# Kernel tuning notes

Hardware: AMD Instinct MI355X
Metric: run time of the kernel (lower is better)

## Reference

```python
import jax, jax.numpy as jnp
import numpy as np

N_Q = 6        # qubits per circuit
N_CL = 32      # entangler layers per circuit
N_MOD = 32     # number of qlayer modules (feature parts)
PART = 64      # 2048 // 32

# Pauli-Z sign table: state flattened as (B, 2**N_Q) with wire 0 the most
# significant axis; signs[k, i] = (-1)**bit_i(k).
_bits = (np.arange(2 ** N_Q)[:, None] >> np.arange(N_Q - 1, -1, -1)[None, :]) & 1
SIGNS = jnp.asarray(1.0 - 2.0 * _bits, dtype=jnp.float32)  # [64, 6]


def _apply_1q(state, gate, wire):
    # state: [B, 2, 2, 2, 2, 2, 2] complex64; gate: [2, 2]
    axis = 1 + wire
    state = jnp.tensordot(gate, state, axes=((1,), (axis,)))
    return jnp.moveaxis(state, 0, axis)


def _apply_cnot(state, ctrl, tgt):
    ci, ti = 1 + ctrl, 1 + tgt
    s0 = jax.lax.index_in_dim(state, 0, ci, keepdims=True)
    s1 = jax.lax.index_in_dim(state, 1, ci, keepdims=True)
    return jnp.concatenate([s0, jnp.flip(s1, axis=ti)], axis=ci)


def _rx(theta):
    c = jnp.cos(theta * 0.5).astype(jnp.complex64)
    s = jnp.sin(theta * 0.5).astype(jnp.complex64)
    return jnp.stack([jnp.stack([c, -1j * s]), jnp.stack([-1j * s, c])])


def _circuit(angles, weights):
    # angles: [B, 6] (AngleEmbedding RY params); weights: [N_CL, 6] (RX params)
    B = angles.shape[0]
    half = angles * 0.5
    # RY(a)|0> = cos(a/2)|0> + sin(a/2)|1>  -> product state
    amps = jnp.stack([jnp.cos(half), jnp.sin(half)], axis=-1).astype(jnp.complex64)  # [B,6,2]
    state = amps[:, 0]
    for q in range(1, N_Q):
        state = state[..., None] * amps[:, q].reshape((B,) + (1,) * q + (2,))
    # state: [B,2,2,2,2,2,2]

    def layer(st, w):
        # BasicEntanglerLayers: RX on every wire, then ring of CNOTs
        for q in range(N_Q):
            st = _apply_1q(st, _rx(w[q]), q)
        for q in range(N_Q):
            st = _apply_cnot(st, q, (q + 1) % N_Q)
        return st, None

    state, _ = jax.lax.scan(jax.checkpoint(layer), state, weights)
    probs = (state.real ** 2 + state.imag ** 2).reshape(B, 2 ** N_Q)
    return probs @ SIGNS  # [B, 6] expvals of PauliZ on each wire


def _forward(features, Wp, bp, qw, Wf, bf):
    B = features.shape[0]
    parts = features.reshape(B, N_MOD, PART)                 # 32 chunks of 64
    angles = jnp.einsum('bpd,qd->bpq', parts, Wp) + bp       # shared projector -> [B,32,6]
    outs = jax.vmap(_circuit, in_axes=(1, 0), out_axes=1)(angles, qw)  # [B,32,6]
    return outs.reshape(B, N_MOD * N_Q) @ Wf.T + bf          # [B, num_classes]


def setup_inputs() -> dict:
    key = jax.random.key(0)
    k1, k2, k3, k4 = jax.random.split(key, 4)
    B, num_classes = 2048, 150
    features = jax.random.normal(k1, (B, 2048), dtype=jnp.float32)
    Wp = jax.random.normal(k2, (N_Q, PART), dtype=jnp.float32) * (1.0 / np.sqrt(PART))
    bp = jnp.zeros((N_Q,), dtype=jnp.float32)
    qw = jax.random.uniform(k3, (N_MOD, N_CL, N_Q), dtype=jnp.float32) * (2.0 * np.pi)
    Wf = jax.random.normal(k4, (num_classes, N_MOD * N_Q), dtype=jnp.float32) * (1.0 / np.sqrt(N_MOD * N_Q))
    bf = jnp.zeros((num_classes,), dtype=jnp.float32)
    return {'features': features, 'Wp': Wp, 'bp': bp, 'qw': qw, 'Wf': Wf, 'bf': bf}


def reference(features, Wp, bp, qw, Wf, bf):
    return _forward(features, Wp, bp, qw, Wf, bf)
```

## Files before the change

kernel.cpp:

```cpp
#include <hip/hip_runtime.h>

#define NQ   6
#define DIM  64
#define NMOD 32
#define NCL  32
#define BATCH 2048
#define NCLS 150
#define KF   192
#define NROWS (BATCH*NMOD)

#define OFF_UT    0
#define OFF_OUTS  262144

__global__ __launch_bounds__(256) void k_prep(const float* __restrict__ qw,
                                              float* __restrict__ UTf) {
    __shared__ float2 csl[NCL * NQ];
    int tid = threadIdx.x;
    int lane = tid & 63;
    int w = tid >> 6;
    int p = blockIdx.x >> 4;
    int col = ((blockIdx.x & 15) << 2) + w;

    if (tid < NCL * NQ) {
        float s, c;
        sincosf(0.5f * qw[p * NCL * NQ + tid], &s, &c);
        csl[tid] = make_float2(c, s);
    }
    __syncthreads();

    int dst = lane;
#pragma unroll
    for (int q = 0; q < NQ; ++q) {
        int cm = 1 << (5 - q), tm = 1 << (5 - ((q + 1) % 6));
        dst ^= (dst & cm) ? tm : 0;
    }
    int dst_b = dst << 2;

    float re = (lane == col) ? 1.f : 0.f;
    float im = 0.f;

    for (int layer = 0; layer < NCL; ++layer) {
#pragma unroll
        for (int q = 0; q < NQ; ++q) {
            float2 cs = csl[layer * NQ + q];
            int mask = 1 << (5 - q);
            float pre = __shfl_xor(re, mask, 64);
            float pim = __shfl_xor(im, mask, 64);
            float nre = fmaf(cs.x, re, cs.y * pim);
            float nim = fmaf(cs.x, im, -cs.y * pre);
            re = nre;
            im = nim;
        }
        re = __int_as_float(__builtin_amdgcn_ds_permute(dst_b, __float_as_int(re)));
        im = __int_as_float(__builtin_amdgcn_ds_permute(dst_b, __float_as_int(im)));
    }
    float2* UT2 = (float2*)UTf;
    UT2[p * (DIM * DIM) + lane * DIM + col] = make_float2(re, im);
}

__global__ __launch_bounds__(256, 4) void k_fused(const float* __restrict__ features,
                                                  const float* __restrict__ Wp,
                                                  const float* __restrict__ bp,
                                                  const float* __restrict__ UTf,
                                                  float* __restrict__ outs) {
    __shared__ float ldsA[64 * 65];
    __shared__ float ldsW[NQ * 64];
    __shared__ float camps_l[64 * 13];
    __shared__ float zl[4][5][64];

    int tid = threadIdx.x;
    int lane = tid & 63;
    int w = tid >> 6;
    int wq = __builtin_amdgcn_readfirstlane(w);
    int p = blockIdx.x & 31;
    int btile = blockIdx.x >> 5;

    {
        int l = tid >> 2;
        int quarter = tid & 3;
        const float* src = features + (size_t)(btile * 64 + l) * 2048 + p * 64
                         + quarter * 16;
        float4 v0 = *(const float4*)(src + 0);
        float4 v1 = *(const float4*)(src + 4);
        float4 v2 = *(const float4*)(src + 8);
        float4 v3 = *(const float4*)(src + 12);
        int d0 = quarter * 16;
        float tmp[16] = {v0.x,v0.y,v0.z,v0.w, v1.x,v1.y,v1.z,v1.w,
                         v2.x,v2.y,v2.z,v2.w, v3.x,v3.y,v3.z,v3.w};
#pragma unroll
        for (int j = 0; j < 16; ++j) ldsA[(d0 + j) * 65 + l] = tmp[j];
        for (int idx = tid; idx < NQ * 64; idx += 256) ldsW[idx] = Wp[idx];
    }
    __syncthreads();

    {
        int l = tid & 63;
        int q0 = tid >> 6;
        float acc0 = 0.f, acc1 = 0.f;
        bool two = (q0 < 2);
        int q1 = q0 + 4;
#pragma unroll
        for (int d = 0; d < 64; ++d) {
            float a = ldsA[d * 65 + l];
            acc0 = fmaf(a, ldsW[q0 * 64 + d], acc0);
            if (two) acc1 = fmaf(a, ldsW[q1 * 64 + d], acc1);
        }
        float s, c;
        sincosf(0.5f * (acc0 + bp[q0]), &s, &c);
        camps_l[l * 13 + 2 * q0 + 0] = c;
        camps_l[l * 13 + 2 * q0 + 1] = s;
        if (two) {
            sincosf(0.5f * (acc1 + bp[q1]), &s, &c);
            camps_l[l * 13 + 2 * q1 + 0] = c;
            camps_l[l * 13 + 2 * q1 + 1] = s;
        }
    }
    __syncthreads();

    float ca[12];
#pragma unroll
    for (int j = 0; j < 12; ++j) ca[j] = camps_l[lane * 13 + j];

    float psi[DIM];
    psi[0] = 1.f;
#pragma unroll
    for (int q = 5; q >= 0; --q) {
        int sz = 1 << (5 - q);
        float c = ca[2 * q], s = ca[2 * q + 1];
#pragma unroll
        for (int k = 0; k < 64; ++k) {
            if (k < sz) {
                psi[k + sz] = psi[k] * s;
                psi[k] = psi[k] * c;
            }
        }
    }

    float ps = 0.f, z2 = 0.f, z3 = 0.f, z4 = 0.f, z5 = 0.f;
    const float4* Ubase = (const float4*)(UTf + (size_t)p * DIM * DIM * 2);

#pragma unroll
    for (int ii = 0; ii < 16; ++ii) {
        int i = wq * 16 + ii;
        const float4* Ur = Ubase + i * 32;
        float yre = 0.f, yim = 0.f;
#pragma unroll
        for (int j4 = 0; j4 < 32; ++j4) {
            float4 u = Ur[j4];
            yre = fmaf(u.x, psi[2 * j4], yre);
            yim = fmaf(u.y, psi[2 * j4], yim);
            yre = fmaf(u.z, psi[2 * j4 + 1], yre);
            yim = fmaf(u.w, psi[2 * j4 + 1], yim);
        }
        float prob = fmaf(yre, yre, yim * yim);
        ps += prob;
        z2 += (ii & 8) ? -prob : prob;
        z3 += (ii & 4) ? -prob : prob;
        z4 += (ii & 2) ? -prob : prob;
        z5 += (ii & 1) ? -prob : prob;
    }

    zl[w][0][lane] = ps;
    zl[w][1][lane] = z2;
    zl[w][2][lane] = z3;
    zl[w][3][lane] = z4;
    zl[w][4][lane] = z5;
    __syncthreads();

    if (tid < 64) {
        float p0 = zl[0][0][tid], p1 = zl[1][0][tid], p2 = zl[2][0][tid], p3 = zl[3][0][tid];
        float z0 = (p0 + p1) - (p2 + p3);
        float z1 = (p0 - p1) + (p2 - p3);
        float o2 = zl[0][1][tid] + zl[1][1][tid] + zl[2][1][tid] + zl[3][1][tid];
        float o3 = zl[0][2][tid] + zl[1][2][tid] + zl[2][2][tid] + zl[3][2][tid];
        float o4 = zl[0][3][tid] + zl[1][3][tid] + zl[2][3][tid] + zl[3][3][tid];
        float o5 = zl[0][4][tid] + zl[1][4][tid] + zl[2][4][tid] + zl[3][4][tid];
        int bb = btile * 64 + tid;
        float* o = outs + (size_t)bb * KF + p * NQ;
        o[0] = z0; o[1] = z1; o[2] = o2; o[3] = o3; o[4] = o4; o[5] = o5;
    }
}

__global__ __launch_bounds__(256) void k_final(const float* __restrict__ outs,
                                               const float* __restrict__ Wf,
                                               const float* __restrict__ bf,
                                               float* __restrict__ out) {
    int tid = threadIdx.x;
    int b = blockIdx.x * 64 + (tid & 63);
    int c = blockIdx.y * 4 + (tid >> 6);
    if (c >= NCLS) return;
    float acc = bf[c];
    const float* orow = outs + (size_t)b * KF;
    const float* wrow = Wf + (size_t)c * KF;
#pragma unroll
    for (int k = 0; k < KF; k += 4) {
        float4 o = *(const float4*)&orow[k];
        float4 wv = *(const float4*)&wrow[k];
        acc = fmaf(o.x, wv.x, acc);
        acc = fmaf(o.y, wv.y, acc);
        acc = fmaf(o.z, wv.z, acc);
        acc = fmaf(o.w, wv.w, acc);
    }
    out[b * NCLS + c] = acc;
}

extern "C" void kernel_launch(void* const* d_in, const int* in_sizes, int n_in,
                              void* d_out, int out_size, void* d_ws, size_t ws_size,
                              hipStream_t stream) {
    const float* features = (const float*)d_in[0];
    const float* Wp       = (const float*)d_in[1];
    const float* bp       = (const float*)d_in[2];
    const float* qw       = (const float*)d_in[3];
    const float* Wf       = (const float*)d_in[4];
    const float* bf       = (const float*)d_in[5];
    float* out = (float*)d_out;
    float* ws  = (float*)d_ws;

    float* UT    = ws + OFF_UT;
    float* outsb = ws + OFF_OUTS;

    k_prep<<<NMOD * 16, 256, 0, stream>>>(qw, UT);
    k_fused<<<NMOD * (BATCH / 64), 256, 0, stream>>>(features, Wp, bp, UT, outsb);
    k_final<<<dim3(BATCH / 64, (NCLS + 3) / 4), 256, 0, stream>>>(outsb, Wf, bf, out);
}
```

Measured before the change: 164.2 us.

## Apply circuit unitary via split-bf16 MFMA instead of scalar FP32 matvec

The precomputed 64x64 complex unitary is now stored as hi/lo bf16 pairs in an MFMA fragment layout. The initial product states are also split into hi/lo bf16 and staged in shared memory, which is unioned with the projection buffers. The state-times-unitary product then runs as 32x32x16 bf16 MFMAs using three-term split products to keep near-FP32 accuracy. This replaces per-lane scalar FMA loops over 64 registers of state. The Pauli-Z reductions are reworked to match the MFMA accumulator layout, at the cost of extra conversion work and a dropped lo*lo term.

```diff
diff --git a/kernel.cpp b/kernel.cpp
--- a/kernel.cpp
+++ b/kernel.cpp
@@ -7,13 +7,14 @@
 #define BATCH 2048
 #define NCLS 150
 #define KF   192
-#define NROWS (BATCH*NMOD)
-
-#define OFF_UT    0
+
 #define OFF_OUTS  262144
 
+typedef short bf16x8 __attribute__((ext_vector_type(8)));
+typedef float f32x16 __attribute__((ext_vector_type(16)));
+
 __global__ __launch_bounds__(256) void k_prep(const float* __restrict__ qw,
-                                              float* __restrict__ UTf) {
+                                              unsigned short* __restrict__ UB) {
     __shared__ float2 csl[NCL * NQ];
     int tid = threadIdx.x;
     int lane = tid & 63;
@@ -38,7 +39,6 @@
 
     float re = (lane == col) ? 1.f : 0.f;
     float im = 0.f;
-
     for (int layer = 0; layer < NCL; ++layer) {
 #pragma unroll
         for (int q = 0; q < NQ; ++q) {
@@ -54,24 +54,39 @@
         re = __int_as_float(__builtin_amdgcn_ds_permute(dst_b, __float_as_int(re)));
         im = __int_as_float(__builtin_amdgcn_ds_permute(dst_b, __float_as_int(im)));
     }
-    float2* UT2 = (float2*)UTf;
-    UT2[p * (DIM * DIM) + lane * DIM + col] = make_float2(re, im);
-}
+
+    int F = (((lane >> 5) * 4 + (col >> 4)) << 9)
+          + (((lane & 31) | (((col >> 3) & 1) << 5)) << 3) + (col & 7);
+    unsigned short* base = UB + (size_t)p * 4 * 4096;
+    unsigned int rb = __float_as_uint(re);
+    float rhf = __uint_as_float(rb & 0xFFFF0000u);
+    unsigned int rlb = __float_as_uint(re - rhf);
+    unsigned int ib = __float_as_uint(im);
+    float ihf = __uint_as_float(ib & 0xFFFF0000u);
+    unsigned int ilb = __float_as_uint(im - ihf);
+    base[0 * 4096 + F] = (unsigned short)(rb >> 16);
+    base[1 * 4096 + F] = (unsigned short)(rlb >> 16);
+    base[2 * 4096 + F] = (unsigned short)(ib >> 16);
+    base[3 * 4096 + F] = (unsigned short)(ilb >> 16);
+}
+
+union SharedU {
+    struct { float A[64 * 65]; float W[NQ * 64]; } s01;
+    struct { unsigned short hi[64 * 72]; unsigned short lo[64 * 72]; } s23;
+};
 
 __global__ __launch_bounds__(256, 4) void k_fused(const float* __restrict__ features,
                                                   const float* __restrict__ Wp,
                                                   const float* __restrict__ bp,
-                                                  const float* __restrict__ UTf,
+                                                  const unsigned short* __restrict__ UB,
                                                   float* __restrict__ outs) {
-    __shared__ float ldsA[64 * 65];
-    __shared__ float ldsW[NQ * 64];
+    __shared__ __align__(16) SharedU sh;
     __shared__ float camps_l[64 * 13];
-    __shared__ float zl[4][5][64];
+    __shared__ float zacc[4][6][32];
 
     int tid = threadIdx.x;
     int lane = tid & 63;
     int w = tid >> 6;
-    int wq = __builtin_amdgcn_readfirstlane(w);
     int p = blockIdx.x & 31;
     int btile = blockIdx.x >> 5;
 
@@ -88,8 +103,8 @@
         float tmp[16] = {v0.x,v0.y,v0.z,v0.w, v1.x,v1.y,v1.z,v1.w,
                          v2.x,v2.y,v2.z,v2.w, v3.x,v3.y,v3.z,v3.w};
 #pragma unroll
-        for (int j = 0; j < 16; ++j) ldsA[(d0 + j) * 65 + l] = tmp[j];
-        for (int idx = tid; idx < NQ * 64; idx += 256) ldsW[idx] = Wp[idx];
+        for (int j = 0; j < 16; ++j) sh.s01.A[(d0 + j) * 65 + l] = tmp[j];
+        for (int idx = tid; idx < NQ * 64; idx += 256) sh.s01.W[idx] = Wp[idx];
     }
     __syncthreads();
 
@@ -101,9 +116,9 @@
         int q1 = q0 + 4;
 #pragma unroll
         for (int d = 0; d < 64; ++d) {
-            float a = ldsA[d * 65 + l];
-            acc0 = fmaf(a, ldsW[q0 * 64 + d], acc0);
-            if (two) acc1 = fmaf(a, ldsW[q1 * 64 + d], acc1);
+            float a = sh.s01.A[d * 65 + l];
+            acc0 = fmaf(a, sh.s01.W[q0 * 64 + d], acc0);
+            if (two) acc1 = fmaf(a, sh.s01.W[q1 * 64 + d], acc1);
         }
         float s, c;
         sincosf(0.5f * (acc0 + bp[q0]), &s, &c);
@@ -117,67 +132,119 @@
     }
     __syncthreads();
 
-    float ca[12];
-#pragma unroll
-    for (int j = 0; j < 12; ++j) ca[j] = camps_l[lane * 13 + j];
-
-    float psi[DIM];
-    psi[0] = 1.f;
-#pragma unroll
-    for (int q = 5; q >= 0; --q) {
-        int sz = 1 << (5 - q);
-        float c = ca[2 * q], s = ca[2 * q + 1];
-#pragma unroll
-        for (int k = 0; k < 64; ++k) {
-            if (k < sz) {
-                psi[k + sz] = psi[k] * s;
-                psi[k] = psi[k] * c;
+    {
+        float ca[12];
+#pragma unroll
+        for (int j = 0; j < 12; ++j) ca[j] = camps_l[lane * 13 + j];
+        float base_[32];
+        base_[0] = 1.f;
+#pragma unroll
+        for (int q = 4; q >= 0; --q) {
+            int sz = 1 << (4 - q);
+            float c = ca[2 * q], s = ca[2 * q + 1];
+#pragma unroll
+            for (int k = 0; k < 32; ++k) {
+                if (k < sz) {
+                    base_[k + sz] = base_[k] * s;
+                    base_[k] = base_[k] * c;
+                }
             }
         }
-    }
-
-    float ps = 0.f, z2 = 0.f, z3 = 0.f, z4 = 0.f, z5 = 0.f;
-    const float4* Ubase = (const float4*)(UTf + (size_t)p * DIM * DIM * 2);
-
-#pragma unroll
-    for (int ii = 0; ii < 16; ++ii) {
-        int i = wq * 16 + ii;
-        const float4* Ur = Ubase + i * 32;
-        float yre = 0.f, yim = 0.f;
-#pragma unroll
-        for (int j4 = 0; j4 < 32; ++j4) {
-            float4 u = Ur[j4];
-            yre = fmaf(u.x, psi[2 * j4], yre);
-            yim = fmaf(u.y, psi[2 * j4], yim);
-            yre = fmaf(u.z, psi[2 * j4 + 1], yre);
-            yim = fmaf(u.w, psi[2 * j4 + 1], yim);
-        }
-        float prob = fmaf(yre, yre, yim * yim);
-        ps += prob;
-        z2 += (ii & 8) ? -prob : prob;
-        z3 += (ii & 4) ? -prob : prob;
-        z4 += (ii & 2) ? -prob : prob;
-        z5 += (ii & 1) ? -prob : prob;
-    }
-
-    zl[w][0][lane] = ps;
-    zl[w][1][lane] = z2;
-    zl[w][2][lane] = z3;
-    zl[w][3][lane] = z4;
-    zl[w][4][lane] = z5;
+        float c5 = ca[10], s5 = ca[11];
+        unsigned int* pHi = (unsigned int*)sh.s23.hi;
+        unsigned int* pLo = (unsigned int*)sh.s23.lo;
+#pragma unroll
+        for (int v = w * 8; v < w * 8 + 8; ++v) {
+            float f0 = base_[v] * c5, f1 = base_[v] * s5;
+            unsigned int b0 = __float_as_uint(f0), b1 = __float_as_uint(f1);
+            unsigned int hi = (b0 >> 16) | (b1 & 0xFFFF0000u);
+            float f0h = __uint_as_float(b0 & 0xFFFF0000u);
+            float f1h = __uint_as_float(b1 & 0xFFFF0000u);
+            unsigned int l0 = __float_as_uint(f0 - f0h);
+            unsigned int l1 = __float_as_uint(f1 - f1h);
+            unsigned int lo = (l0 >> 16) | (l1 & 0xFFFF0000u);
+            pHi[lane * 36 + v] = hi;
+            pLo[lane * 36 + v] = lo;
+        }
+    }
+    __syncthreads();
+
+    int mi = w >> 1, nb = w & 1;
+    int h = lane >> 5;
+    int bloc = nb * 32 + (lane & 31);
+    f32x16 accR, accI;
+#pragma unroll
+    for (int r = 0; r < 16; ++r) { accR[r] = 0.f; accI[r] = 0.f; }
+
+    const unsigned short* Af = UB + (size_t)p * 16384 + ((mi * 4) << 9) + (lane << 3);
+#pragma unroll
+    for (int t = 0; t < 4; ++t) {
+        const unsigned short* fp = Af + (t << 9);
+        bf16x8 aRH = *(const bf16x8*)(fp + 0 * 4096);
+        bf16x8 aRL = *(const bf16x8*)(fp + 1 * 4096);
+        bf16x8 aIH = *(const bf16x8*)(fp + 2 * 4096);
+        bf16x8 aIL = *(const bf16x8*)(fp + 3 * 4096);
+        const unsigned short* bh = sh.s23.hi + bloc * 72 + t * 16 + 8 * h;
+        const unsigned short* bl = sh.s23.lo + bloc * 72 + t * 16 + 8 * h;
+        bf16x8 bH = *(const bf16x8*)bh;
+        bf16x8 bL = *(const bf16x8*)bl;
+        accR = __builtin_amdgcn_mfma_f32_32x32x16_bf16(aRH, bH, accR, 0, 0, 0);
+        accR = __builtin_amdgcn_mfma_f32_32x32x16_bf16(aRH, bL, accR, 0, 0, 0);
+        accR = __builtin_amdgcn_mfma_f32_32x32x16_bf16(aRL, bH, accR, 0, 0, 0);
+        accI = __builtin_amdgcn_mfma_f32_32x32x16_bf16(aIH, bH, accI, 0, 0, 0);
+        accI = __builtin_amdgcn_mfma_f32_32x32x16_bf16(aIH, bL, accI, 0, 0, 0);
+        accI = __builtin_amdgcn_mfma_f32_32x32x16_bf16(aIL, bH, accI, 0, 0, 0);
+    }
+
+    {
+        float pr[16];
+#pragma unroll
+        for (int r = 0; r < 16; ++r)
+            pr[r] = fmaf(accR[r], accR[r], accI[r] * accI[r]);
+
+        float zA = 0.f, z1 = 0.f, z2 = 0.f, z4 = 0.f, z5 = 0.f;
+#pragma unroll
+        for (int g = 0; g < 4; ++g) {
+            float r0 = pr[4 * g], r1 = pr[4 * g + 1], r2 = pr[4 * g + 2], r3 = pr[4 * g + 3];
+            float a  = (r0 + r1) + (r2 + r3);
+            float s5 = (r0 - r1) + (r2 - r3);
+            float s4 = (r0 + r1) - (r2 + r3);
+            zA += a;
+            z2 += (g & 1) ? -a : a;
+            z1 += (g & 2) ? -a : a;
+            z5 += s5;
+            z4 += s4;
+        }
+        float tA = __shfl_xor(zA, 32, 64);
+        float z3 = h ? (tA - zA) : (zA - tA);
+        zA += tA;
+        z1 += __shfl_xor(z1, 32, 64);
+        z2 += __shfl_xor(z2, 32, 64);
+        z4 += __shfl_xor(z4, 32, 64);
+        z5 += __shfl_xor(z5, 32, 64);
+
+        if (lane < 32) {
+            zacc[w][0][lane] = zA;
+            zacc[w][1][lane] = z1;
+            zacc[w][2][lane] = z2;
+            zacc[w][3][lane] = z3;
+            zacc[w][4][lane] = z4;
+            zacc[w][5][lane] = z5;
+        }
+    }
     __syncthreads();
 
     if (tid < 64) {
-        float p0 = zl[0][0][tid], p1 = zl[1][0][tid], p2 = zl[2][0][tid], p3 = zl[3][0][tid];
-        float z0 = (p0 + p1) - (p2 + p3);
-        float z1 = (p0 - p1) + (p2 - p3);
-        float o2 = zl[0][1][tid] + zl[1][1][tid] + zl[2][1][tid] + zl[3][1][tid];
-        float o3 = zl[0][2][tid] + zl[1][2][tid] + zl[2][2][tid] + zl[3][2][tid];
-        float o4 = zl[0][3][tid] + zl[1][3][tid] + zl[2][3][tid] + zl[3][3][tid];
-        float o5 = zl[0][4][tid] + zl[1][4][tid] + zl[2][4][tid] + zl[3][4][tid];
-        int bb = btile * 64 + tid;
-        float* o = outs + (size_t)bb * KF + p * NQ;
-        o[0] = z0; o[1] = z1; o[2] = o2; o[3] = o3; o[4] = o4; o[5] = o5;
+        int nb2 = tid >> 5, c = tid & 31;
+        int wA = nb2, wB = 2 + nb2;
+        float z0 = zacc[wA][0][c] - zacc[wB][0][c];
+        float o1 = zacc[wA][1][c] + zacc[wB][1][c];
+        float o2 = zacc[wA][2][c] + zacc[wB][2][c];
+        float o3 = zacc[wA][3][c] + zacc[wB][3][c];
+        float o4 = zacc[wA][4][c] + zacc[wB][4][c];
+        float o5 = zacc[wA][5][c] + zacc[wB][5][c];
+        float* o = outs + (size_t)(btile * 64 + tid) * KF + p * NQ;
+        o[0] = z0; o[1] = o1; o[2] = o2; o[3] = o3; o[4] = o4; o[5] = o5;
     }
 }
 
@@ -216,10 +283,10 @@
     float* out = (float*)d_out;
     float* ws  = (float*)d_ws;
 
-    float* UT    = ws + OFF_UT;
+    unsigned short* UB = (unsigned short*)ws;
     float* outsb = ws + OFF_OUTS;
 
-    k_prep<<<NMOD * 16, 256, 0, stream>>>(qw, UT);
-    k_fused<<<NMOD * (BATCH / 64), 256, 0, stream>>>(features, Wp, bp, UT, outsb);
+    k_prep<<<NMOD * 16, 256, 0, stream>>>(qw, UB);
+    k_fused<<<NMOD * (BATCH / 64), 256, 0, stream>>>(features, Wp, bp, UB, outsb);
     k_final<<<dim3(BATCH / 64, (NCLS + 3) / 4), 256, 0, stream>>>(outsb, Wf, bf, out);
 }
```

Result: faster. 133.1 us (-18.9%).
